# Kernel optimization log

Measured on AMD Instinct MI355X. Metric: run time of the kernel, lower is better.

Reference implementation:

```python
import jax, jax.numpy as jnp
import numpy as np

N, D, E, K = 8192, 256, 262144, 8


def _linear_params(key, fan_in, fan_out):
    kw, kb = jax.random.split(key)
    s = 1.0 / np.sqrt(fan_in)
    W = jax.random.uniform(kw, (fan_in, fan_out), jnp.float32, -s, s)
    b = jax.random.uniform(kb, (fan_out,), jnp.float32, -s, s)
    return W, b


def setup_inputs() -> dict:
    key = jax.random.key(0)
    ks = jax.random.split(key, 8)
    enc = jax.random.normal(ks[0], (N, D), jnp.float32)
    edge_index = jax.random.randint(ks[1], (2, E), 0, N, jnp.int64)
    edge_attr = jax.random.uniform(ks[2], (E,), jnp.float32)
    ADJ = jax.random.bernoulli(ks[3], 32.0 / N, (N, N)).astype(jnp.float32)
    eps = jax.random.normal(ks[4], (N, K, D), jnp.float32)  # randn_like noise
    W1, b1 = _linear_params(ks[5], 2 * D, D)
    W2, b2 = _linear_params(ks[6], 2 * D, D)
    W3, b3 = _linear_params(ks[7], D, D)
    W4, b4 = _linear_params(jax.random.fold_in(key, 99), D, D)
    return dict(enc=enc, edge_index=edge_index, edge_attr=edge_attr, ADJ=ADJ,
                eps=eps, W1=W1, b1=b1, W2=W2, b2=b2, W3=W3, b3=b3, W4=W4, b4=b4)


def _simple_conv_cat(x, src, dst, w):
    # PyG SimpleConv(aggr='mean', combine_root='cat'):
    # weighted messages from src, mean-aggregated at dst, concat [root, agg]
    msg = x[src] * w[:, None]                                   # [E, D]
    agg = jax.ops.segment_sum(msg, dst, num_segments=N)         # [N, D]
    cnt = jax.ops.segment_sum(jnp.ones_like(w), dst, num_segments=N)
    agg = agg / jnp.maximum(cnt, 1.0)[:, None]
    return jnp.concatenate([x, agg], axis=-1)                   # [N, 2D]


def reference(enc, edge_index, edge_attr, ADJ, eps, W1, b1, W2, b2, W3, b3, W4, b4):
    src, dst = edge_index[0], edge_index[1]  # flow: source -> target
    # GNN: two SimpleConv + Linear + ReLU blocks
    h = _simple_conv_cat(enc, src, dst, edge_attr)
    h = jax.nn.relu(h @ W1 + b1)
    h = _simple_conv_cat(h, src, dst, edge_attr)
    h = jax.nn.relu(h @ W2 + b2)
    enc2 = h + enc
    mu = (enc2 @ W3 + b3)[:, None, :]                            # [N,1,D] -> broadcast K
    log_var = (enc2 @ W4 + b4)[:, None, :]
    mu = jnp.broadcast_to(mu, (N, K, D))
    log_var = jnp.broadcast_to(log_var, (N, K, D))
    Z = mu + eps * jnp.exp(0.5 * log_var)                        # [N,K,D]
    kl = -0.5 * jnp.mean(jnp.sum(1.0 + log_var - mu ** 2 - jnp.exp(log_var), axis=-1))
    Z_l = Z.mean(axis=1)                                         # [N,D]
    logits = Z_l @ Z_l.T                                         # [N,N]
    graph_loss = jnp.mean(jax.nn.softplus(logits) - logits * ADJ)  # BCEWithLogits
    vae_loss = kl + graph_loss
    return enc2, Z, vae_loss
```

## Files before the change

kernel.cpp:

```cpp
#include <hip/hip_runtime.h>

#define NN 8192
#define DD 256
#define EE 262144

typedef __attribute__((ext_vector_type(8))) short bf16x8;
typedef __attribute__((ext_vector_type(4))) float f32x4;

static __device__ __forceinline__ unsigned short f2b(float x) {
  unsigned int u = __float_as_uint(x);
  u += 0x7fffu + ((u >> 16) & 1u);
  return (unsigned short)(u >> 16);
}
static __device__ __forceinline__ float b2f(unsigned short u) {
  return __uint_as_float(((unsigned int)u) << 16);
}

__global__ void k_prep(const float* __restrict__ enc,
                       const float* __restrict__ W1, const float* __restrict__ W2,
                       const float* __restrict__ W3, const float* __restrict__ W4,
                       const float* __restrict__ b3, const float* __restrict__ b4,
                       unsigned short* __restrict__ encb,
                       unsigned short* __restrict__ W1t, unsigned short* __restrict__ W2t,
                       unsigned short* __restrict__ W34t, float* __restrict__ b34,
                       int* __restrict__ cnt, int* __restrict__ fill,
                       double* __restrict__ sums, int* __restrict__ ticket,
                       int* __restrict__ nnz) {
  int idx = blockIdx.x * 256 + threadIdx.x;
  {
    float4 v = ((const float4*)enc)[idx];
    ushort4 o;
    o.x = f2b(v.x); o.y = f2b(v.y); o.z = f2b(v.z); o.w = f2b(v.w);
    ((ushort4*)encb)[idx] = o;
  }
  if (idx < 512 * 256) {
    int k = idx >> 8, n = idx & 255;
    W1t[n * 512 + k] = f2b(W1[idx]);
    W2t[n * 512 + k] = f2b(W2[idx]);
  }
  if (idx < 256 * 512) {
    int k = idx >> 9, n = idx & 511;
    float v = (n < 256) ? W3[k * 256 + n] : W4[k * 256 + (n - 256)];
    W34t[n * 256 + k] = f2b(v);
  }
  if (idx < 512) b34[idx] = (idx < 256) ? b3[idx] : b4[idx - 256];
  if (idx < NN) cnt[idx] = 0;
  else if (idx < 2 * NN) fill[idx - NN] = 0;
  else if (idx < 2 * NN + 4) sums[idx - 2 * NN] = 0.0;
  else if (idx == 2 * NN + 4) *ticket = 0;
  else if (idx == 2 * NN + 5) *nnz = 0;
}

__global__ void k_count(const int* __restrict__ dst, int* __restrict__ cnt) {
  int e = blockIdx.x * 256 + threadIdx.x;
  if (e < EE) atomicAdd(&cnt[dst[e]], 1);
}

__global__ void k_scan(const int* __restrict__ cnt, int* __restrict__ row_ptr) {
  __shared__ int s[1024];
  int t = threadIdx.x;
  int loc[8]; int tot = 0;
#pragma unroll
  for (int i = 0; i < 8; ++i) { loc[i] = cnt[t * 8 + i]; tot += loc[i]; }
  s[t] = tot; __syncthreads();
  for (int off = 1; off < 1024; off <<= 1) {
    int v = s[t];
    int add = (t >= off) ? s[t - off] : 0;
    __syncthreads();
    s[t] = v + add;
    __syncthreads();
  }
  int run = (t == 0) ? 0 : s[t - 1];
#pragma unroll
  for (int i = 0; i < 8; ++i) { row_ptr[t * 8 + i] = run; run += loc[i]; }
  if (t == 1023) row_ptr[NN] = run;
}

__global__ void k_fill(const int* __restrict__ dst, const int* __restrict__ src,
                       const float* __restrict__ w, const int* __restrict__ row_ptr,
                       int* __restrict__ fill, int* __restrict__ slist,
                       float* __restrict__ wlist) {
  int e = blockIdx.x * 256 + threadIdx.x;
  if (e < EE) {
    int d = dst[e];
    int idx = atomicAdd(&fill[d], 1);
    int pos = row_ptr[d] + idx;
    slist[pos] = src[e];
    wlist[pos] = w[e];
  }
}

__global__ __launch_bounds__(256) void k_conv(const unsigned short* __restrict__ xb,
                                              const int* __restrict__ slist,
                                              const float* __restrict__ wlist,
                                              const int* __restrict__ row_ptr,
                                              unsigned short* __restrict__ out) {
  int tid = threadIdx.x, wid = tid >> 6, lane = tid & 63;
  int n = blockIdx.x * 4 + wid;
  const ushort4* x4 = (const ushort4*)xb;
  float ax = 0.f, ay = 0.f, az = 0.f, aw = 0.f;
  int b = row_ptr[n], e2 = row_ptr[n + 1];
  int i = b;
  for (; i + 1 < e2; i += 2) {
    int s0 = slist[i], s1 = slist[i + 1];
    float w0 = wlist[i], w1 = wlist[i + 1];
    ushort4 v0 = x4[(size_t)s0 * 64 + lane];
    ushort4 v1 = x4[(size_t)s1 * 64 + lane];
    ax += b2f(v0.x) * w0 + b2f(v1.x) * w1;
    ay += b2f(v0.y) * w0 + b2f(v1.y) * w1;
    az += b2f(v0.z) * w0 + b2f(v1.z) * w1;
    aw += b2f(v0.w) * w0 + b2f(v1.w) * w1;
  }
  if (i < e2) {
    int s0 = slist[i];
    float w0 = wlist[i];
    ushort4 v0 = x4[(size_t)s0 * 64 + lane];
    ax += b2f(v0.x) * w0; ay += b2f(v0.y) * w0;
    az += b2f(v0.z) * w0; aw += b2f(v0.w) * w0;
  }
  float inv = 1.0f / fmaxf((float)(e2 - b), 1.0f);
  ushort4 rv = x4[(size_t)n * 64 + lane];
  ushort4 av;
  av.x = f2b(ax * inv); av.y = f2b(ay * inv);
  av.z = f2b(az * inv); av.w = f2b(aw * inv);
  *(ushort4*)&out[(size_t)n * 512 + lane * 4]       = rv;
  *(ushort4*)&out[(size_t)n * 512 + 256 + lane * 4] = av;
}

static __device__ __forceinline__ void gemm_core(const unsigned short* __restrict__ A,
                                                 const unsigned short* __restrict__ BT,
                                                 int K, int m0, int n0,
                                                 unsigned short* As, unsigned short* Bs,
                                                 f32x4 acc[4][4]) {
  const int tid = threadIdx.x;
  const int lane = tid & 63, wid = tid >> 6;
  const int wr = wid >> 1, wc = wid & 1;
  const int r16 = lane & 15, g = lane >> 4;
  for (int kt = 0; kt < K; kt += 64) {
    __syncthreads();
#pragma unroll
    for (int j = 0; j < 4; ++j) {
      int c = tid + j * 256;
      int row = c >> 3, slot = c & 7;
      int sw = (slot ^ (row & 7)) << 3;
      *(bf16x8*)&As[row * 64 + sw] = *(const bf16x8*)&A[(size_t)(m0 + row) * K + kt + slot * 8];
      *(bf16x8*)&Bs[row * 64 + sw] = *(const bf16x8*)&BT[(size_t)(n0 + row) * K + kt + slot * 8];
    }
    __syncthreads();
#pragma unroll
    for (int kk = 0; kk < 64; kk += 32) {
      bf16x8 av[4], bv[4];
      int bslot = (kk >> 3) + g;
#pragma unroll
      for (int m = 0; m < 4; ++m) {
        int row = wr * 64 + m * 16 + r16;
        av[m] = *(const bf16x8*)&As[row * 64 + ((bslot ^ (row & 7)) << 3)];
      }
#pragma unroll
      for (int n2 = 0; n2 < 4; ++n2) {
        int row = wc * 64 + n2 * 16 + r16;
        bv[n2] = *(const bf16x8*)&Bs[row * 64 + ((bslot ^ (row & 7)) << 3)];
      }
#pragma unroll
      for (int m = 0; m < 4; ++m)
#pragma unroll
        for (int n2 = 0; n2 < 4; ++n2)
          acc[m][n2] = __builtin_amdgcn_mfma_f32_16x16x32_bf16(av[m], bv[n2], acc[m][n2], 0, 0, 0);
    }
  }
}

template <bool RELU, bool RESID, bool WC, bool WB>
__global__ __launch_bounds__(256) void k_gemm(const unsigned short* __restrict__ A,
                                              const unsigned short* __restrict__ BT,
                                              const float* __restrict__ bias,
                                              const float* __restrict__ resid,
                                              float* __restrict__ C,
                                              unsigned short* __restrict__ Cb,
                                              int K, int Ncols) {
  __shared__ unsigned short As[128 * 64];
  __shared__ unsigned short Bs[128 * 64];
  f32x4 acc[4][4] = {};
  int m0 = blockIdx.x * 128, n0 = blockIdx.y * 128;
  gemm_core(A, BT, K, m0, n0, As, Bs, acc);
  const int tid = threadIdx.x;
  const int lane = tid & 63, wid = tid >> 6;
  const int wr = wid >> 1, wc = wid & 1;
  const int r16 = lane & 15, g = lane >> 4;
#pragma unroll
  for (int m = 0; m < 4; ++m)
#pragma unroll
    for (int rr = 0; rr < 4; ++rr) {
      int grow = m0 + wr * 64 + m * 16 + g * 4 + rr;
#pragma unroll
      for (int n2 = 0; n2 < 4; ++n2) {
        int gcol = n0 + wc * 64 + n2 * 16 + r16;
        float v = acc[m][n2][rr] + bias[gcol];
        if (RELU) v = fmaxf(v, 0.f);
        if (RESID) v += resid[(size_t)grow * Ncols + gcol];
        if (WC) C[(size_t)grow * Ncols + gcol] = v;
        if (WB) Cb[(size_t)grow * Ncols + gcol] = f2b(v);
      }
    }
}

__global__ __launch_bounds__(256) void k_logits(const unsigned short* __restrict__ Zl,
                                                double* __restrict__ sp_sum) {
  int bx = blockIdx.x, by = blockIdx.y;
  if (by < bx) return;
  __shared__ unsigned short As[128 * 64];
  __shared__ unsigned short Bs[128 * 64];
  f32x4 acc[4][4] = {};
  gemm_core(Zl, Zl, 256, bx * 128, by * 128, As, Bs, acc);
  const int tid = threadIdx.x;
  float lsum = 0.f;
#pragma unroll
  for (int m = 0; m < 4; ++m)
#pragma unroll
    for (int rr = 0; rr < 4; ++rr)
#pragma unroll
      for (int n2 = 0; n2 < 4; ++n2) {
        float c = acc[m][n2][rr];
        lsum += fmaxf(c, 0.f) + __logf(1.0f + __expf(-fabsf(c)));
      }
  lsum *= (bx == by) ? 1.0f : 2.0f;
  __syncthreads();
  float* red = (float*)As;
  red[tid] = lsum;
  __syncthreads();
  for (int off = 128; off > 0; off >>= 1) {
    if (tid < off) red[tid] += red[tid + off];
    __syncthreads();
  }
  if (tid == 0) atomicAdd(sp_sum, (double)red[0]);
}

#define CMP_BLOCKS 1024
#define CMP_CAP 1024
__global__ __launch_bounds__(256) void k_compact(const float* __restrict__ ADJ,
                                                 int* __restrict__ nnz,
                                                 unsigned int* __restrict__ eidx) {
  __shared__ unsigned int sidx[CMP_CAP];
  __shared__ int scnt, sbase;
  if (threadIdx.x == 0) scnt = 0;
  __syncthreads();
  const float4* a4 = (const float4*)ADJ;
  size_t base = (size_t)blockIdx.x * 16384;
#pragma unroll 4
  for (int k = 0; k < 64; ++k) {
    size_t c = base + (size_t)k * 256 + threadIdx.x;
    float4 a = a4[c];
    unsigned int idx0 = (unsigned int)(c * 4);
#pragma unroll
    for (int u = 0; u < 4; ++u) {
      if ((&a.x)[u] != 0.f) {
        int p = atomicAdd(&scnt, 1);
        if (p < CMP_CAP) sidx[p] = idx0 + u;
      }
    }
  }
  __syncthreads();
  if (threadIdx.x == 0) {
    int c = scnt; if (c > CMP_CAP) c = CMP_CAP;
    sbase = atomicAdd(nnz, c);
    scnt = c;
  }
  __syncthreads();
  int cnt = scnt, gb = sbase;
  for (int t = threadIdx.x; t < cnt; t += 256) eidx[gb + t] = sidx[t];
}

#define EDGE_BLOCKS 512
__global__ __launch_bounds__(256) void k_edge(const unsigned short* __restrict__ Zl,
                                              const int* __restrict__ nnz,
                                              const unsigned int* __restrict__ eidx,
                                              double* __restrict__ sums,
                                              int* __restrict__ ticket,
                                              float* __restrict__ out_loss) {
  const int tid = threadIdx.x, wid = tid >> 6, lane = tid & 63;
  const int n = *nnz;
  const ushort4* z4 = (const ushort4*)Zl;
  float accum = 0.f;
  const int wstride = EDGE_BLOCKS * 4;
  for (int e = blockIdx.x * 4 + wid; e < n; e += wstride) {
    unsigned int id = eidx[e];
    int i = id >> 13, j = id & (NN - 1);
    ushort4 a = z4[(size_t)i * 64 + lane];
    ushort4 b = z4[(size_t)j * 64 + lane];
    accum += b2f(a.x) * b2f(b.x) + b2f(a.y) * b2f(b.y) +
             b2f(a.z) * b2f(b.z) + b2f(a.w) * b2f(b.w);
  }
#pragma unroll
  for (int off = 32; off > 0; off >>= 1) accum += __shfl_down(accum, off, 64);
  __shared__ float red[4];
  if (lane == 0) red[wid] = accum;
  __syncthreads();
  if (tid == 0) {
    atomicAdd(&sums[2], (double)(red[0] + red[1] + red[2] + red[3]));
    __threadfence();
    int old = atomicAdd(ticket, 1);
    if (old == EDGE_BLOCKS - 1) {
      double kl_s  = atomicAdd(&sums[0], 0.0);
      double sp_s  = atomicAdd(&sums[1], 0.0);
      double dot_s = atomicAdd(&sums[2], 0.0);
      double kl = -0.5 * kl_s / (double)NN;
      double gl = (sp_s - dot_s) / ((double)NN * (double)NN);
      out_loss[0] = (float)(kl + gl);
    }
  }
}

__global__ __launch_bounds__(256) void k_z(const float* __restrict__ mulv,
                                           const float* __restrict__ eps,
                                           float* __restrict__ Zout,
                                           unsigned short* __restrict__ Zl,
                                           double* __restrict__ kl_sum) {
  int tid = threadIdx.x, wid = tid >> 6, lane = tid & 63;
  int n = blockIdx.x * 4 + wid;
  const float4* m4 = (const float4*)mulv;
  float4 mu = m4[(size_t)n * 128 + lane];
  float4 lv = m4[(size_t)n * 128 + 64 + lane];
  float4 sig;
  sig.x = __expf(0.5f * lv.x); sig.y = __expf(0.5f * lv.y);
  sig.z = __expf(0.5f * lv.z); sig.w = __expf(0.5f * lv.w);
  const float4* e4 = (const float4*)eps;
  float4* z4 = (float4*)Zout;
  float esx = 0.f, esy = 0.f, esz = 0.f, esw = 0.f;
#pragma unroll
  for (int k = 0; k < 8; ++k) {
    size_t idx = ((size_t)n * 8 + k) * 64 + lane;
    float4 e = e4[idx];
    float4 z;
    z.x = mu.x + e.x * sig.x; z.y = mu.y + e.y * sig.y;
    z.z = mu.z + e.z * sig.z; z.w = mu.w + e.w * sig.w;
    z4[idx] = z;
    esx += e.x; esy += e.y; esz += e.z; esw += e.w;
  }
  ushort4 zl;
  zl.x = f2b(mu.x + sig.x * esx * 0.125f);
  zl.y = f2b(mu.y + sig.y * esy * 0.125f);
  zl.z = f2b(mu.z + sig.z * esz * 0.125f);
  zl.w = f2b(mu.w + sig.w * esw * 0.125f);
  *(ushort4*)&Zl[(size_t)n * 256 + lane * 4] = zl;
  float t = (1.0f + lv.x - mu.x * mu.x - sig.x * sig.x)
          + (1.0f + lv.y - mu.y * mu.y - sig.y * sig.y)
          + (1.0f + lv.z - mu.z * mu.z - sig.z * sig.z)
          + (1.0f + lv.w - mu.w * mu.w - sig.w * sig.w);
#pragma unroll
  for (int off = 32; off > 0; off >>= 1) t += __shfl_down(t, off, 64);
  __shared__ float red[4];
  if (lane == 0) red[wid] = t;
  __syncthreads();
  if (tid == 0) atomicAdd(kl_sum, (double)(red[0] + red[1] + red[2] + red[3]));
}

extern "C" void kernel_launch(void* const* d_in, const int* in_sizes, int n_in,
                              void* d_out, int out_size, void* d_ws, size_t ws_size,
                              hipStream_t stream) {
  const float* enc = (const float*)d_in[0];
  const int*   ei  = (const int*)d_in[1];
  const int*   src = ei;
  const int*   dst = ei + EE;
  const float* w   = (const float*)d_in[2];
  const float* ADJ = (const float*)d_in[3];
  const float* eps = (const float*)d_in[4];
  const float* W1  = (const float*)d_in[5];
  const float* b1  = (const float*)d_in[6];
  const float* W2  = (const float*)d_in[7];
  const float* b2  = (const float*)d_in[8];
  const float* W3  = (const float*)d_in[9];
  const float* b3  = (const float*)d_in[10];
  const float* W4  = (const float*)d_in[11];
  const float* b4  = (const float*)d_in[12];

  char* ws = (char*)d_ws;
  size_t off = 0;
  auto alloc = [&](size_t bytes) -> void* {
    void* p = ws + off;
    off = (off + bytes + 255) & ~(size_t)255;
    return p;
  };
  unsigned short* h1b   = (unsigned short*)alloc((size_t)NN * 512 * 2);
  unsigned short* hb    = (unsigned short*)alloc((size_t)NN * 256 * 2);
  float*          mulv  = (float*)alloc((size_t)NN * 512 * 4);
  unsigned short* enc2b = (unsigned short*)alloc((size_t)NN * 256 * 2);
  unsigned short* Zlb   = (unsigned short*)alloc((size_t)NN * 256 * 2);
  unsigned short* encb  = (unsigned short*)alloc((size_t)NN * 256 * 2);
  unsigned short* W1t   = (unsigned short*)alloc(512 * 256 * 2);
  unsigned short* W2t   = (unsigned short*)alloc(512 * 256 * 2);
  unsigned short* W34t  = (unsigned short*)alloc(512 * 256 * 2);
  float*          b34v  = (float*)alloc(512 * 4);
  int*            cnt   = (int*)alloc(NN * 4);
  int*            row_ptr = (int*)alloc((NN + 1) * 4);
  int*            fill  = (int*)alloc(NN * 4);
  int*            slist = (int*)alloc((size_t)EE * 4);
  float*          wlist = (float*)alloc((size_t)EE * 4);
  unsigned int*   eidx  = (unsigned int*)alloc((size_t)2097152 * 4);
  double*         sums  = (double*)alloc(32);
  int*            ticket = (int*)alloc(16);
  int*            nnz    = (int*)alloc(16);

  float* out_enc2 = (float*)d_out;
  float* out_Z    = out_enc2 + (size_t)NN * 256;
  float* out_loss = out_Z + (size_t)NN * 8 * 256;

  k_prep<<<2048, 256, 0, stream>>>(enc, W1, W2, W3, W4, b3, b4, encb, W1t, W2t, W34t,
                                   b34v, cnt, fill, sums, ticket, nnz);
  k_count<<<EE / 256, 256, 0, stream>>>(dst, cnt);
  k_scan<<<1, 1024, 0, stream>>>(cnt, row_ptr);
  k_fill<<<EE / 256, 256, 0, stream>>>(dst, src, w, row_ptr, fill, slist, wlist);

  k_conv<<<NN / 4, 256, 0, stream>>>(encb, slist, wlist, row_ptr, h1b);
  k_gemm<true, false, false, true><<<dim3(64, 2), 256, 0, stream>>>(h1b, W1t, b1, nullptr, nullptr, hb, 512, 256);
  k_conv<<<NN / 4, 256, 0, stream>>>(hb, slist, wlist, row_ptr, h1b);
  k_gemm<true, true, true, true><<<dim3(64, 2), 256, 0, stream>>>(h1b, W2t, b2, enc, out_enc2, enc2b, 512, 256);
  k_gemm<false, false, true, false><<<dim3(64, 4), 256, 0, stream>>>(enc2b, W34t, b34v, nullptr, mulv, nullptr, 256, 512);
  k_z<<<NN / 4, 256, 0, stream>>>(mulv, eps, out_Z, Zlb, sums);
  k_compact<<<CMP_BLOCKS, 256, 0, stream>>>(ADJ, nnz, eidx);
  k_logits<<<dim3(64, 64), 256, 0, stream>>>(Zlb, sums + 1);
  k_edge<<<EDGE_BLOCKS, 256, 0, stream>>>(Zlb, nnz, eidx, sums, ticket, out_loss);
}
```

Before: 708.0 us.

## Fuse ADJ compaction with logits GEMM and unroll gather loops by four

Merges the ADJ compaction kernel and the symmetric logits softplus GEMM into a single launch with block-ID dispatch. The memory-bound ADJ scan can then overlap with the compute-bound GEMM tiles instead of running serially. It also unrolls the neighbor gather in the conv kernel and the edge dot-product loop by four, putting more independent loads in flight. The fused kernel's shared memory is sized for the GEMM tiles, which may lower occupancy for the compaction blocks.

Result: faster. 665.8 us (-6.0%).

```diff
diff --git a/kernel.cpp b/kernel.cpp
--- a/kernel.cpp
+++ b/kernel.cpp
@@ -14,6 +14,10 @@
 }
 static __device__ __forceinline__ float b2f(unsigned short u) {
   return __uint_as_float(((unsigned int)u) << 16);
+}
+static __device__ __forceinline__ float dot4(ushort4 a, ushort4 b) {
+  return b2f(a.x) * b2f(b.x) + b2f(a.y) * b2f(b.y) +
+         b2f(a.z) * b2f(b.z) + b2f(a.w) * b2f(b.w);
 }
 
 __global__ void k_prep(const float* __restrict__ enc,
@@ -101,17 +105,19 @@
   float ax = 0.f, ay = 0.f, az = 0.f, aw = 0.f;
   int b = row_ptr[n], e2 = row_ptr[n + 1];
   int i = b;
-  for (; i + 1 < e2; i += 2) {
-    int s0 = slist[i], s1 = slist[i + 1];
-    float w0 = wlist[i], w1 = wlist[i + 1];
+  for (; i + 3 < e2; i += 4) {
+    int s0 = slist[i], s1 = slist[i + 1], s2 = slist[i + 2], s3 = slist[i + 3];
+    float w0 = wlist[i], w1 = wlist[i + 1], w2 = wlist[i + 2], w3 = wlist[i + 3];
     ushort4 v0 = x4[(size_t)s0 * 64 + lane];
     ushort4 v1 = x4[(size_t)s1 * 64 + lane];
-    ax += b2f(v0.x) * w0 + b2f(v1.x) * w1;
-    ay += b2f(v0.y) * w0 + b2f(v1.y) * w1;
-    az += b2f(v0.z) * w0 + b2f(v1.z) * w1;
-    aw += b2f(v0.w) * w0 + b2f(v1.w) * w1;
-  }
-  if (i < e2) {
+    ushort4 v2 = x4[(size_t)s2 * 64 + lane];
+    ushort4 v3 = x4[(size_t)s3 * 64 + lane];
+    ax += b2f(v0.x) * w0 + b2f(v1.x) * w1 + b2f(v2.x) * w2 + b2f(v3.x) * w3;
+    ay += b2f(v0.y) * w0 + b2f(v1.y) * w1 + b2f(v2.y) * w2 + b2f(v3.y) * w3;
+    az += b2f(v0.z) * w0 + b2f(v1.z) * w1 + b2f(v2.z) * w2 + b2f(v3.z) * w3;
+    aw += b2f(v0.w) * w0 + b2f(v1.w) * w1 + b2f(v2.w) * w2 + b2f(v3.w) * w3;
+  }
+  for (; i < e2; ++i) {
     int s0 = slist[i];
     float w0 = wlist[i];
     ushort4 v0 = x4[(size_t)s0 * 64 + lane];
@@ -204,70 +210,74 @@
     }
 }
 
-__global__ __launch_bounds__(256) void k_logits(const unsigned short* __restrict__ Zl,
-                                                double* __restrict__ sp_sum) {
-  int bx = blockIdx.x, by = blockIdx.y;
-  if (by < bx) return;
+#define CMP_BLOCKS 1024
+#define CMP_CAP 1024
+__global__ __launch_bounds__(256) void k_fused(const float* __restrict__ ADJ,
+                                               const unsigned short* __restrict__ Zl,
+                                               int* __restrict__ nnz,
+                                               unsigned int* __restrict__ eidx,
+                                               double* __restrict__ sp_sum) {
   __shared__ unsigned short As[128 * 64];
   __shared__ unsigned short Bs[128 * 64];
-  f32x4 acc[4][4] = {};
-  gemm_core(Zl, Zl, 256, bx * 128, by * 128, As, Bs, acc);
+  __shared__ int scnt, sbase;
+  const int bid = blockIdx.x;
   const int tid = threadIdx.x;
-  float lsum = 0.f;
-#pragma unroll
-  for (int m = 0; m < 4; ++m)
-#pragma unroll
-    for (int rr = 0; rr < 4; ++rr)
-#pragma unroll
-      for (int n2 = 0; n2 < 4; ++n2) {
-        float c = acc[m][n2][rr];
-        lsum += fmaxf(c, 0.f) + __logf(1.0f + __expf(-fabsf(c)));
+
+  if (bid < CMP_BLOCKS) {
+    unsigned int* sidx = (unsigned int*)As;
+    if (tid == 0) scnt = 0;
+    __syncthreads();
+    const float4* a4 = (const float4*)ADJ;
+    size_t base = (size_t)bid * 16384;
+#pragma unroll 8
+    for (int k = 0; k < 64; ++k) {
+      size_t c = base + (size_t)k * 256 + tid;
+      float4 a = a4[c];
+      unsigned int idx0 = (unsigned int)(c * 4);
+#pragma unroll
+      for (int u = 0; u < 4; ++u) {
+        if ((&a.x)[u] != 0.f) {
+          int p = atomicAdd(&scnt, 1);
+          if (p < CMP_CAP) sidx[p] = idx0 + u;
+        }
       }
-  lsum *= (bx == by) ? 1.0f : 2.0f;
-  __syncthreads();
-  float* red = (float*)As;
-  red[tid] = lsum;
-  __syncthreads();
-  for (int off = 128; off > 0; off >>= 1) {
-    if (tid < off) red[tid] += red[tid + off];
-    __syncthreads();
-  }
-  if (tid == 0) atomicAdd(sp_sum, (double)red[0]);
-}
-
-#define CMP_BLOCKS 1024
-#define CMP_CAP 1024
-__global__ __launch_bounds__(256) void k_compact(const float* __restrict__ ADJ,
-                                                 int* __restrict__ nnz,
-                                                 unsigned int* __restrict__ eidx) {
-  __shared__ unsigned int sidx[CMP_CAP];
-  __shared__ int scnt, sbase;
-  if (threadIdx.x == 0) scnt = 0;
-  __syncthreads();
-  const float4* a4 = (const float4*)ADJ;
-  size_t base = (size_t)blockIdx.x * 16384;
-#pragma unroll 4
-  for (int k = 0; k < 64; ++k) {
-    size_t c = base + (size_t)k * 256 + threadIdx.x;
-    float4 a = a4[c];
-    unsigned int idx0 = (unsigned int)(c * 4);
-#pragma unroll
-    for (int u = 0; u < 4; ++u) {
-      if ((&a.x)[u] != 0.f) {
-        int p = atomicAdd(&scnt, 1);
-        if (p < CMP_CAP) sidx[p] = idx0 + u;
-      }
-    }
-  }
-  __syncthreads();
-  if (threadIdx.x == 0) {
-    int c = scnt; if (c > CMP_CAP) c = CMP_CAP;
-    sbase = atomicAdd(nnz, c);
-    scnt = c;
-  }
-  __syncthreads();
-  int cnt = scnt, gb = sbase;
-  for (int t = threadIdx.x; t < cnt; t += 256) eidx[gb + t] = sidx[t];
+    }
+    __syncthreads();
+    if (tid == 0) {
+      int c = scnt; if (c > CMP_CAP) c = CMP_CAP;
+      sbase = atomicAdd(nnz, c);
+      scnt = c;
+    }
+    __syncthreads();
+    int cnt = scnt, gb = sbase;
+    for (int t = tid; t < cnt; t += 256) eidx[gb + t] = sidx[t];
+  } else {
+    int lin = bid - CMP_BLOCKS;
+    int bx = lin & 63, by = lin >> 6;
+    if (by < bx) return;
+    f32x4 acc[4][4] = {};
+    gemm_core(Zl, Zl, 256, bx * 128, by * 128, As, Bs, acc);
+    float lsum = 0.f;
+#pragma unroll
+    for (int m = 0; m < 4; ++m)
+#pragma unroll
+      for (int rr = 0; rr < 4; ++rr)
+#pragma unroll
+        for (int n2 = 0; n2 < 4; ++n2) {
+          float c = acc[m][n2][rr];
+          lsum += fmaxf(c, 0.f) + __logf(1.0f + __expf(-fabsf(c)));
+        }
+    lsum *= (bx == by) ? 1.0f : 2.0f;
+    __syncthreads();
+    float* red = (float*)As;
+    red[tid] = lsum;
+    __syncthreads();
+    for (int off = 128; off > 0; off >>= 1) {
+      if (tid < off) red[tid] += red[tid + off];
+      __syncthreads();
+    }
+    if (tid == 0) atomicAdd(sp_sum, (double)red[0]);
+  }
 }
 
 #define EDGE_BLOCKS 512
@@ -281,14 +291,21 @@
   const int n = *nnz;
   const ushort4* z4 = (const ushort4*)Zl;
   float accum = 0.f;
-  const int wstride = EDGE_BLOCKS * 4;
-  for (int e = blockIdx.x * 4 + wid; e < n; e += wstride) {
+  const int stride = EDGE_BLOCKS * 4 * 4;
+  int e = (blockIdx.x * 4 + wid) * 4;
+  for (; e + 3 < n; e += stride) {
+    unsigned int i0 = eidx[e], i1 = eidx[e + 1], i2 = eidx[e + 2], i3 = eidx[e + 3];
+    ushort4 a0 = z4[(size_t)(i0 >> 13) * 64 + lane], b0 = z4[(size_t)(i0 & (NN - 1)) * 64 + lane];
+    ushort4 a1 = z4[(size_t)(i1 >> 13) * 64 + lane], b1 = z4[(size_t)(i1 & (NN - 1)) * 64 + lane];
+    ushort4 a2 = z4[(size_t)(i2 >> 13) * 64 + lane], b2 = z4[(size_t)(i2 & (NN - 1)) * 64 + lane];
+    ushort4 a3 = z4[(size_t)(i3 >> 13) * 64 + lane], b3 = z4[(size_t)(i3 & (NN - 1)) * 64 + lane];
+    accum += dot4(a0, b0) + dot4(a1, b1) + dot4(a2, b2) + dot4(a3, b3);
+  }
+  for (int q = 0; q < 3 && e < n; ++q, ++e) {
     unsigned int id = eidx[e];
-    int i = id >> 13, j = id & (NN - 1);
-    ushort4 a = z4[(size_t)i * 64 + lane];
-    ushort4 b = z4[(size_t)j * 64 + lane];
-    accum += b2f(a.x) * b2f(b.x) + b2f(a.y) * b2f(b.y) +
-             b2f(a.z) * b2f(b.z) + b2f(a.w) * b2f(b.w);
+    ushort4 a = z4[(size_t)(id >> 13) * 64 + lane];
+    ushort4 b = z4[(size_t)(id & (NN - 1)) * 64 + lane];
+    accum += dot4(a, b);
   }
 #pragma unroll
   for (int off = 32; off > 0; off >>= 1) accum += __shfl_down(accum, off, 64);
@@ -416,7 +433,6 @@
   k_gemm<true, true, true, true><<<dim3(64, 2), 256, 0, stream>>>(h1b, W2t, b2, enc, out_enc2, enc2b, 512, 256);
   k_gemm<false, false, true, false><<<dim3(64, 4), 256, 0, stream>>>(enc2b, W34t, b34v, nullptr, mulv, nullptr, 256, 512);
   k_z<<<NN / 4, 256, 0, stream>>>(mulv, eps, out_Z, Zlb, sums);
-  k_compact<<<CMP_BLOCKS, 256, 0, stream>>>(ADJ, nnz, eidx);
-  k_logits<<<dim3(64, 64), 256, 0, stream>>>(Zlb, sums + 1);
+  k_fused<<<CMP_BLOCKS + 4096, 256, 0, stream>>>(ADJ, Zlb, nnz, eidx, sums + 1);
   k_edge<<<EDGE_BLOCKS, 256, 0, stream>>>(Zlb, nnz, eidx, sums, ticket, out_loss);
 }
```
